# Performance work log

Measured on AMD Instinct MI355X. Metric: run time of the kernel, lower is better.

Reference implementation:

```python
import jax, jax.numpy as jnp
import numpy as np

B, T, IN_DIM, HID, H, L = 64, 256, 4096, 1024, 8, 2
HD = HID // H
K_TASK, K_ADP, OUT_DIM = 64, 1, 12
EPS = 1e-5


def _ln(x, g, b):
    m = x.mean(-1, keepdims=True)
    v = ((x - m) ** 2).mean(-1, keepdims=True)
    return (x - m) * jax.lax.rsqrt(v + EPS) * g + b


def _rope_tables(t_len, hd, base=10000.0):
    inv = 1.0 / base ** (jnp.arange(0, hd, 2, dtype=jnp.float32) / hd)
    freqs = jnp.arange(t_len, dtype=jnp.float32)[:, None] * inv[None, :]
    emb = jnp.concatenate([freqs, freqs], axis=-1)  # (T, hd)
    return jnp.cos(emb), jnp.sin(emb)


def _rotate_half(x):
    x1, x2 = x[..., ::2], x[..., 1::2]
    return jnp.stack((-x2, x1), axis=-1).reshape(x.shape)


def _apply_rope(q, k, cos, sin):
    cos = cos[None, None]
    sin = sin[None, None]
    return q * cos + _rotate_half(q) * sin, k * cos + _rotate_half(k) * sin


def _block(x, h_a_i, h_t_i, p, Wq, bq, Wks, bks, Wvs, bvs, Wka, bka, Wva, bva,
           Wkt, bkt, Wvt, bvt, Wo, bo, g, fg, fb, Wf, bff):
    Bx, Tx, C = x.shape
    gv = jnp.tanh(g)
    h_ad = jnp.concatenate([h_a_i, p], axis=1)  # (B, K_ADP+1, HID)
    cos, sin = _rope_tables(Tx, HD)

    def heads(t):
        return t.reshape(Bx, -1, H, HD).transpose(0, 2, 1, 3)

    q = heads(x @ Wq.T + bq)
    ks = heads(x @ Wks.T + bks)
    vs = heads(x @ Wvs.T + bvs)
    q, ks = _apply_rope(q, ks, cos, sin)
    ka = heads(h_ad @ Wka.T + bka)
    va = heads(h_ad @ Wva.T + bva)
    kt = heads(h_t_i @ Wkt.T + bkt)
    vt = heads(h_t_i @ Wvt.T + bvt)
    s_self = jnp.einsum('bhtd,bhsd->bhts', q, ks)
    s_ad = jnp.einsum('bhtd,bhsd->bhts', q, ka)
    s_tk = jnp.einsum('bhtd,bhsd->bhts', q, kt) * gv
    scores = jnp.concatenate([s_self, s_ad, s_tk], axis=-1) / np.float32(np.sqrt(HD))
    attn = jax.nn.softmax(scores, axis=-1)
    v_all = jnp.concatenate([vs, va, vt], axis=2)
    out = jnp.einsum('bhts,bhsd->bhtd', attn, v_all)
    out = out.transpose(0, 2, 1, 3).reshape(Bx, Tx, C)
    out = out @ Wo.T + bo
    return jax.nn.relu(_ln(out + x, fg, fb) @ Wf.T + bff)


def setup_inputs() -> dict:
    key = jax.random.key(0)
    kit = iter(jax.random.split(key, 64))
    def n(shape, s=0.02):
        return jax.random.normal(next(kit), shape, jnp.float32) * s
    return dict(
        x=jax.random.normal(next(kit), (B, T, IN_DIM), jnp.float32),
        h_a=jax.random.normal(next(kit), (B, L, K_ADP, HID), jnp.float32),
        h_t=jax.random.normal(next(kit), (B, L, K_TASK, HID), jnp.float32),
        p=jax.random.normal(next(kit), (B, 1, HID), jnp.float32),
        ln1_g=jnp.ones((IN_DIM,), jnp.float32), ln1_b=jnp.zeros((IN_DIM,), jnp.float32),
        W1=n((HID, IN_DIM)), b1=jnp.zeros((HID,), jnp.float32),
        Wq=n((L, HID, HID)), bq=jnp.zeros((L, HID), jnp.float32),
        Wks=n((L, HID, HID)), bks=jnp.zeros((L, HID), jnp.float32),
        Wvs=n((L, HID, HID)), bvs=jnp.zeros((L, HID), jnp.float32),
        Wka=n((L, HID, HID)), bka=jnp.zeros((L, HID), jnp.float32),
        Wva=n((L, HID, HID)), bva=jnp.zeros((L, HID), jnp.float32),
        Wkt=n((L, HID, HID)), bkt=jnp.zeros((L, HID), jnp.float32),
        Wvt=n((L, HID, HID)), bvt=jnp.zeros((L, HID), jnp.float32),
        Wo=n((L, HID, HID)), bo=jnp.zeros((L, HID), jnp.float32),
        gate=jnp.full((L,), 0.1, jnp.float32),
        fln_g=jnp.ones((L, HID), jnp.float32), fln_b=jnp.zeros((L, HID), jnp.float32),
        Wf=n((L, HID, HID)), bf=jnp.zeros((L, HID), jnp.float32),
        ln2_g=jnp.ones((HID,), jnp.float32), ln2_b=jnp.zeros((HID,), jnp.float32),
        W2=n((OUT_DIM, HID)), b2=jnp.zeros((OUT_DIM,), jnp.float32),
    )


def reference(x, h_a, h_t, p, ln1_g, ln1_b, W1, b1, Wq, bq, Wks, bks, Wvs, bvs,
              Wka, bka, Wva, bva, Wkt, bkt, Wvt, bvt, Wo, bo, gate, fln_g, fln_b,
              Wf, bf, ln2_g, ln2_b, W2, b2):
    h = _ln(x, ln1_g, ln1_b)
    h = jax.nn.relu(h @ W1.T + b1)  # (B, T, HID)
    for i in range(L):
        h = _block(h, h_a[:, i], h_t[:, i], p,
                   Wq[i], bq[i], Wks[i], bks[i], Wvs[i], bvs[i],
                   Wka[i], bka[i], Wva[i], bva[i], Wkt[i], bkt[i],
                   Wvt[i], bvt[i], Wo[i], bo[i], gate[i],
                   fln_g[i], fln_b[i], Wf[i], bf[i])
    h = _ln(h, ln2_g, ln2_b)
    return h @ W2.T + b2
```

## Files before the change

### kernel.cpp

```cpp
#include <hip/hip_runtime.h>
#include <hip/hip_bf16.h>
#include <cstdio>

typedef __hip_bfloat16 bf16;
typedef __attribute__((ext_vector_type(8))) short bf16x8;
typedef __attribute__((ext_vector_type(4))) float f32x4;

constexpr int NB = 64, NT = 256, NIN = 4096, NHID = 1024, NHEAD = 8, NHD = 128;
constexpr int NLAYER = 2, NKT = 64, NKEYS = 322, NOUT = 12;

__device__ __forceinline__ float bf2f(bf16 v) { return __bfloat162float(v); }
__device__ __forceinline__ bf16 f2bf(float v) { return __float2bfloat16(v); }

__device__ __forceinline__ void gload16(const void* g, void* l) {
  __builtin_amdgcn_global_load_lds((const __attribute__((address_space(1))) void*)g,
                                   (__attribute__((address_space(3))) void*)l, 16, 0, 0);
}

template <int OMODE, bool RELU>
__global__ __launch_bounds__(256) void gemm_bt(
    const bf16* __restrict__ A, const bf16* __restrict__ W,
    const float* __restrict__ bias, float* __restrict__ Cf,
    bf16* __restrict__ Cb, int M, int N, int K) {
  __shared__ bf16 As[128 * 32];
  __shared__ bf16 Bs[128 * 32];
  const int tid = threadIdx.x;
  const int wave = tid >> 6, lane = tid & 63;
  const int m0 = blockIdx.x * 128, n0 = blockIdx.y * 128;
  const int wm = (wave >> 1) * 64, wn = (wave & 1) * 64;
  const int lr = lane >> 4, lc = lane & 15;

  f32x4 acc[4][4];
#pragma unroll
  for (int i = 0; i < 4; ++i)
#pragma unroll
    for (int j = 0; j < 4; ++j) acc[i][j] = (f32x4){0.f, 0.f, 0.f, 0.f};

  for (int k0 = 0; k0 < K; k0 += 32) {
#pragma unroll
    for (int j = 0; j < 2; ++j) {
      const int c = (wave * 2 + j) * 64 + lane;
      const int row = c >> 2, kq = (c & 3) * 8;
      gload16(A + (size_t)(m0 + row) * K + k0 + kq, (char*)As + (size_t)(wave * 2 + j) * 1024);
      gload16(W + (size_t)(n0 + row) * K + k0 + kq, (char*)Bs + (size_t)(wave * 2 + j) * 1024);
    }
    __syncthreads();
    bf16x8 af[4], bv[4];
#pragma unroll
    for (int mi = 0; mi < 4; ++mi)
      af[mi] = *(const bf16x8*)(As + (wm + mi * 16 + lc) * 32 + lr * 8);
#pragma unroll
    for (int ni = 0; ni < 4; ++ni)
      bv[ni] = *(const bf16x8*)(Bs + (wn + ni * 16 + lc) * 32 + lr * 8);
#pragma unroll
    for (int mi = 0; mi < 4; ++mi)
#pragma unroll
      for (int ni = 0; ni < 4; ++ni)
        acc[mi][ni] = __builtin_amdgcn_mfma_f32_16x16x32_bf16(af[mi], bv[ni], acc[mi][ni], 0, 0, 0);
    __syncthreads();
  }

#pragma unroll
  for (int mi = 0; mi < 4; ++mi)
#pragma unroll
    for (int ni = 0; ni < 4; ++ni) {
      const int col = n0 + wn + ni * 16 + lc;
      const float bb = bias[col];
#pragma unroll
      for (int i = 0; i < 4; ++i) {
        const int row = m0 + wm + mi * 16 + lr * 4 + i;
        float v = acc[mi][ni][i] + bb;
        if (RELU) v = fmaxf(v, 0.f);
        if constexpr (OMODE == 0 || OMODE == 2) Cf[(size_t)row * N + col] = v;
        if constexpr (OMODE == 1 || OMODE == 2) Cb[(size_t)row * N + col] = f2bf(v);
      }
    }
}

template <int DIM, bool RES, bool OUTBF>
__global__ __launch_bounds__(256) void ln_kernel(
    const float* __restrict__ X, const float* __restrict__ R,
    const float* __restrict__ g, const float* __restrict__ bt,
    bf16* __restrict__ ob, float* __restrict__ of) {
  constexpr int PT = DIM / 1024;
  const int row = blockIdx.x, tid = threadIdx.x;
  const float4* xr = (const float4*)(X + (size_t)row * DIM);
  float4 v[PT];
  float s = 0.f, sq = 0.f;
#pragma unroll
  for (int j = 0; j < PT; ++j) {
    v[j] = xr[tid + j * 256];
    if constexpr (RES) {
      const float4 r4 = ((const float4*)(R + (size_t)row * DIM))[tid + j * 256];
      v[j].x += r4.x; v[j].y += r4.y; v[j].z += r4.z; v[j].w += r4.w;
    }
    s += v[j].x + v[j].y + v[j].z + v[j].w;
    sq += v[j].x * v[j].x + v[j].y * v[j].y + v[j].z * v[j].z + v[j].w * v[j].w;
  }
#pragma unroll
  for (int o = 32; o; o >>= 1) { s += __shfl_down(s, o); sq += __shfl_down(sq, o); }
  __shared__ float red[8];
  const int wave = tid >> 6, lane = tid & 63;
  if (!lane) { red[wave] = s; red[wave + 4] = sq; }
  __syncthreads();
  s = red[0] + red[1] + red[2] + red[3];
  sq = red[4] + red[5] + red[6] + red[7];
  const float mean = s * (1.f / DIM);
  const float var = sq * (1.f / DIM) - mean * mean;
  const float rs = rsqrtf(var + 1e-5f);
#pragma unroll
  for (int j = 0; j < PT; ++j) {
    const int c = (tid + j * 256) * 4;
    const float o0 = (v[j].x - mean) * rs * g[c + 0] + bt[c + 0];
    const float o1 = (v[j].y - mean) * rs * g[c + 1] + bt[c + 1];
    const float o2 = (v[j].z - mean) * rs * g[c + 2] + bt[c + 2];
    const float o3 = (v[j].w - mean) * rs * g[c + 3] + bt[c + 3];
    if constexpr (OUTBF) {
      union { bf16 h[4]; uint2 u; } t;
      t.h[0] = f2bf(o0); t.h[1] = f2bf(o1); t.h[2] = f2bf(o2); t.h[3] = f2bf(o3);
      ((uint2*)(ob + (size_t)row * DIM))[tid + j * 256] = t.u;
    } else {
      float4 w4 = {o0, o1, o2, o3};
      ((float4*)(of + (size_t)row * DIM))[tid + j * 256] = w4;
    }
  }
}

__global__ __launch_bounds__(256) void rope_tables(float* __restrict__ cT,
                                                   float* __restrict__ sT) {
  const int idx = blockIdx.x * 256 + threadIdx.x;
  if (idx >= NT * NHD) return;
  const int t = idx >> 7, d = idx & 127;
  const float inv = powf(10000.f, -(float)(d & 63) / 64.f);
  const float f = (float)t * inv;
  cT[idx] = cosf(f);
  sT[idx] = sinf(f);
}

__global__ __launch_bounds__(256) void rope_apply(bf16* __restrict__ q, bf16* __restrict__ k,
                                                  const float* __restrict__ cT,
                                                  const float* __restrict__ sT) {
  const int idx = blockIdx.x * 256 + threadIdx.x;
  const int i = idx & 63;
  const int hh = (idx >> 6) & 7;
  const int row = idx >> 9;
  const int t = row & (NT - 1);
  const size_t off = (size_t)row * NHID + hh * NHD + i * 2;
  const float c0 = cT[t * NHD + 2 * i], c1 = cT[t * NHD + 2 * i + 1];
  const float s0 = sT[t * NHD + 2 * i], s1 = sT[t * NHD + 2 * i + 1];
  union P2 { unsigned u; bf16 h[2]; };
  P2 a, o;
  a.u = *(const unsigned*)(q + off);
  float x0 = bf2f(a.h[0]), x1 = bf2f(a.h[1]);
  o.h[0] = f2bf(x0 * c0 - x1 * s0);
  o.h[1] = f2bf(x1 * c1 + x0 * s1);
  *(unsigned*)(q + off) = o.u;
  a.u = *(const unsigned*)(k + off);
  x0 = bf2f(a.h[0]); x1 = bf2f(a.h[1]);
  o.h[0] = f2bf(x0 * c0 - x1 * s0);
  o.h[1] = f2bf(x1 * c1 + x0 * s1);
  *(unsigned*)(k + off) = o.u;
}

__global__ __launch_bounds__(256) void attn_mfma(
    const bf16* __restrict__ qb, const bf16* __restrict__ ksb,
    const bf16* __restrict__ vsb, const bf16* __restrict__ kab,
    const bf16* __restrict__ vab, const bf16* __restrict__ ktb,
    const bf16* __restrict__ vtb, const float* __restrict__ gate, int layer,
    bf16* __restrict__ out) {
  __shared__ char Ks[64 * 256];
  __shared__ char Vts[128 * 128];
  __shared__ bf16 Pl[4][16][72];
  const int tid = threadIdx.x;
  const int w = tid >> 6, lane = tid & 63;
  const int lr = lane >> 4, lc = lane & 15;
  const int bid = blockIdx.x;
  const int qc = bid & 3, h = (bid >> 2) & 7, b = bid >> 5;
  const int q0 = qc * 64 + w * 16;
  const float gv = tanhf(gate[layer]);
  const float scale = 0.08838834764831845f;

  bf16x8 af[4];
#pragma unroll
  for (int ks_ = 0; ks_ < 4; ++ks_)
    af[ks_] = *(const bf16x8*)(qb + (size_t)(b * NT + q0 + lc) * NHID + h * NHD +
                               ks_ * 32 + lr * 8);

  f32x4 o[8];
#pragma unroll
  for (int n2 = 0; n2 < 8; ++n2) o[n2] = (f32x4){0.f, 0.f, 0.f, 0.f};
  float m_[4] = {-1e30f, -1e30f, -1e30f, -1e30f};
  float l_[4] = {0.f, 0.f, 0.f, 0.f};

  for (int kb = 0; kb < 6; ++kb) {
#pragma unroll
    for (int i = 0; i < 4; ++i) {
      const int c = tid + i * 256;
      const int key = c >> 4, d0 = (c & 15) * 8;
      const int gk = kb * 64 + key;
      const bf16 *ksrc, *vsrc;
      if (gk < 256) {
        const size_t r = (size_t)(b * NT + gk) * NHID;
        ksrc = ksb + r; vsrc = vsb + r;
      } else if (gk < 258) {
        const size_t r = (size_t)(b * 2 + (gk - 256)) * NHID;
        ksrc = kab + r; vsrc = vab + r;
      } else if (gk < NKEYS) {
        const size_t r = (size_t)(b * NKT + (gk - 258)) * NHID;
        ksrc = ktb + r; vsrc = vtb + r;
      } else {
        const size_t r = (size_t)(b * NT) * NHID;
        ksrc = ksb + r; vsrc = vsb + r;
      }
      const uint4 kv_ = *(const uint4*)(ksrc + h * NHD + d0);
      const uint4 vv_ = *(const uint4*)(vsrc + h * NHD + d0);
      *(uint4*)(Ks + key * 256 + ((d0 * 2) ^ ((key & 7) << 4))) = kv_;
      union { uint4 u; bf16 hh[8]; } t;
      t.u = vv_;
#pragma unroll
      for (int j = 0; j < 8; ++j) {
        const int d = d0 + j;
        *(bf16*)(Vts + d * 128 + ((key * 2) ^ ((d & 7) << 4))) = t.hh[j];
      }
    }
    __syncthreads();

    f32x4 s_[4];
#pragma unroll
    for (int n = 0; n < 4; ++n) s_[n] = (f32x4){0.f, 0.f, 0.f, 0.f};
#pragma unroll
    for (int n = 0; n < 4; ++n) {
      const int row = n * 16 + lc;
#pragma unroll
      for (int ks_ = 0; ks_ < 4; ++ks_) {
        const bf16x8 bk =
            *(const bf16x8*)(Ks + row * 256 + ((ks_ * 64 + lr * 16) ^ ((row & 7) << 4)));
        s_[n] = __builtin_amdgcn_mfma_f32_16x16x32_bf16(af[ks_], bk, s_[n], 0, 0, 0);
      }
    }
#pragma unroll
    for (int n = 0; n < 4; ++n) {
      const int gk = kb * 64 + n * 16 + lc;
      const float f = scale * (gk >= 258 ? gv : 1.f);
#pragma unroll
      for (int i = 0; i < 4; ++i)
        s_[n][i] = (gk >= NKEYS) ? -1e30f : s_[n][i] * f;
    }

    float corr[4];
#pragma unroll
    for (int i = 0; i < 4; ++i) {
      float mx = fmaxf(fmaxf(s_[0][i], s_[1][i]), fmaxf(s_[2][i], s_[3][i]));
#pragma unroll
      for (int off = 8; off; off >>= 1) mx = fmaxf(mx, __shfl_xor(mx, off));
      const float mnew = fmaxf(m_[i], mx);
      corr[i] = __expf(m_[i] - mnew);
      m_[i] = mnew;
      float rs = 0.f;
#pragma unroll
      for (int n = 0; n < 4; ++n) {
        const float p = __expf(s_[n][i] - mnew);
        s_[n][i] = p;
        rs += p;
      }
#pragma unroll
      for (int off = 8; off; off >>= 1) rs += __shfl_xor(rs, off);
      l_[i] = l_[i] * corr[i] + rs;
#pragma unroll
      for (int n = 0; n < 4; ++n) Pl[w][lr * 4 + i][n * 16 + lc] = f2bf(s_[n][i]);
    }
#pragma unroll
    for (int n2 = 0; n2 < 8; ++n2)
#pragma unroll
      for (int i = 0; i < 4; ++i) o[n2][i] *= corr[i];

    asm volatile("s_waitcnt lgkmcnt(0)" ::: "memory");

    const bf16x8 pa0 = *(const bf16x8*)(&Pl[w][lc][lr * 8]);
    const bf16x8 pa1 = *(const bf16x8*)(&Pl[w][lc][32 + lr * 8]);
#pragma unroll
    for (int n2 = 0; n2 < 8; ++n2) {
      const int row = n2 * 16 + lc;
      const bf16x8 bv0 =
          *(const bf16x8*)(Vts + row * 128 + ((lr * 16) ^ ((row & 7) << 4)));
      const bf16x8 bv1 =
          *(const bf16x8*)(Vts + row * 128 + ((64 + lr * 16) ^ ((row & 7) << 4)));
      o[n2] = __builtin_amdgcn_mfma_f32_16x16x32_bf16(pa0, bv0, o[n2], 0, 0, 0);
      o[n2] = __builtin_amdgcn_mfma_f32_16x16x32_bf16(pa1, bv1, o[n2], 0, 0, 0);
    }
    __syncthreads();
  }

#pragma unroll
  for (int i = 0; i < 4; ++i) {
    const float inv = 1.f / l_[i];
    bf16* op = out + (size_t)(b * NT + q0 + lr * 4 + i) * NHID + h * NHD;
#pragma unroll
    for (int n2 = 0; n2 < 8; ++n2) op[n2 * 16 + lc] = f2bf(o[n2][i] * inv);
  }
}

__global__ __launch_bounds__(256) void head_kernel(const float* __restrict__ lnf,
                                                   const float* __restrict__ W2,
                                                   const float* __restrict__ b2,
                                                   float* __restrict__ out) {
  __shared__ float4 xs[4096];
  const int r0 = blockIdx.x * 16;
  const float4* src = (const float4*)(lnf + (size_t)r0 * NHID);
  for (int e = threadIdx.x; e < 4096; e += 256) {
    const int row = e >> 8, c4 = e & 255;
    xs[c4 * 16 + row] = src[e];
  }
  __syncthreads();
  if (threadIdx.x < 192) {
    const int rr = threadIdx.x / 12, n = threadIdx.x % 12;
    const float4* w4 = (const float4*)(W2 + (size_t)n * NHID);
    float s = b2[n];
    for (int k = 0; k < 256; ++k) {
      const float4 a = xs[k * 16 + rr], w = w4[k];
      s += a.x * w.x + a.y * w.y + a.z * w.z + a.w * w.w;
    }
    out[(size_t)(r0 + rr) * NOUT + n] = s;
  }
}

__global__ __launch_bounds__(256) void cvt_f32_bf16(const float* __restrict__ in,
                                                    bf16* __restrict__ o, int n4) {
  const int i = blockIdx.x * 256 + threadIdx.x;
  if (i >= n4) return;
  const float4 v = ((const float4*)in)[i];
  union { bf16 h[4]; uint2 u; } t;
  t.h[0] = f2bf(v.x); t.h[1] = f2bf(v.y); t.h[2] = f2bf(v.z); t.h[3] = f2bf(v.w);
  ((uint2*)o)[i] = t.u;
}

__global__ __launch_bounds__(256) void cvt_ht(const float* __restrict__ ht, int layer,
                                              bf16* __restrict__ o) {
  const int i = blockIdx.x * 256 + threadIdx.x;
  if (i >= NB * NKT * NHID / 4) return;
  const int c4 = i & 255;
  const int s = (i >> 8) & 63;
  const int bb = i >> 14;
  const float4 v =
      ((const float4*)(ht + ((size_t)((bb * NLAYER + layer) * NKT + s)) * NHID))[c4];
  union { bf16 h[4]; uint2 u; } t;
  t.h[0] = f2bf(v.x); t.h[1] = f2bf(v.y); t.h[2] = f2bf(v.z); t.h[3] = f2bf(v.w);
  ((uint2*)o)[i] = t.u;
}

__global__ __launch_bounds__(256) void build_had(const float* __restrict__ ha,
                                                 const float* __restrict__ p, int layer,
                                                 bf16* __restrict__ o) {
  const int i = blockIdx.x * 256 + threadIdx.x;
  if (i >= NB * 2 * NHID / 4) return;
  const int c4 = i & 255;
  const int s = (i >> 8) & 1;
  const int bb = i >> 9;
  const float* base = s ? (p + (size_t)bb * NHID) : (ha + (size_t)(bb * NLAYER + layer) * NHID);
  const float4 v = ((const float4*)base)[c4];
  union { bf16 h[4]; uint2 u; } t;
  t.h[0] = f2bf(v.x); t.h[1] = f2bf(v.y); t.h[2] = f2bf(v.z); t.h[3] = f2bf(v.w);
  ((uint2*)o)[i] = t.u;
}

extern "C" void kernel_launch(void* const* d_in, const int* in_sizes, int n_in,
                              void* d_out, int out_size, void* d_ws, size_t ws_size,
                              hipStream_t stream) {
  const float* x = (const float*)d_in[0];
  const float* h_a = (const float*)d_in[1];
  const float* h_t = (const float*)d_in[2];
  const float* p = (const float*)d_in[3];
  const float* ln1g = (const float*)d_in[4];
  const float* ln1b = (const float*)d_in[5];
  const float* W1 = (const float*)d_in[6];
  const float* b1 = (const float*)d_in[7];
  const float* Wq = (const float*)d_in[8];
  const float* bq = (const float*)d_in[9];
  const float* Wks = (const float*)d_in[10];
  const float* bks = (const float*)d_in[11];
  const float* Wvs = (const float*)d_in[12];
  const float* bvs = (const float*)d_in[13];
  const float* Wka = (const float*)d_in[14];
  const float* bka = (const float*)d_in[15];
  const float* Wva = (const float*)d_in[16];
  const float* bva = (const float*)d_in[17];
  const float* Wkt = (const float*)d_in[18];
  const float* bkt = (const float*)d_in[19];
  const float* Wvt = (const float*)d_in[20];
  const float* bvt = (const float*)d_in[21];
  const float* Wo = (const float*)d_in[22];
  const float* bo = (const float*)d_in[23];
  const float* gate = (const float*)d_in[24];
  const float* flng = (const float*)d_in[25];
  const float* flnb = (const float*)d_in[26];
  const float* Wf = (const float*)d_in[27];
  const float* bff = (const float*)d_in[28];
  const float* ln2g = (const float*)d_in[29];
  const float* ln2b = (const float*)d_in[30];
  const float* W2 = (const float*)d_in[31];
  const float* b2 = (const float*)d_in[32];

  char* wsp = (char*)d_ws;
  size_t off = 0;
  auto alloc = [&](size_t bytes) -> void* {
    void* rp = wsp + off;
    off = (off + bytes + 255) & ~(size_t)255;
    return rp;
  };
  const size_t MT = (size_t)NB * NT;

  bf16* W1b = (bf16*)alloc((size_t)NHID * NIN * 2);
  bf16* Wqb = (bf16*)alloc((size_t)NLAYER * NHID * NHID * 2);
  bf16* Wksb = (bf16*)alloc((size_t)NLAYER * NHID * NHID * 2);
  bf16* Wvsb = (bf16*)alloc((size_t)NLAYER * NHID * NHID * 2);
  bf16* Wkab = (bf16*)alloc((size_t)NLAYER * NHID * NHID * 2);
  bf16* Wvab = (bf16*)alloc((size_t)NLAYER * NHID * NHID * 2);
  bf16* Wktb = (bf16*)alloc((size_t)NLAYER * NHID * NHID * 2);
  bf16* Wvtb = (bf16*)alloc((size_t)NLAYER * NHID * NHID * 2);
  bf16* Wob = (bf16*)alloc((size_t)NLAYER * NHID * NHID * 2);
  bf16* Wfb = (bf16*)alloc((size_t)NLAYER * NHID * NHID * 2);
  float* ropeC = (float*)alloc((size_t)NT * NHD * 4);
  float* ropeS = (float*)alloc((size_t)NT * NHD * 4);
  float* hF = (float*)alloc(MT * NHID * 4);
  bf16* hB = (bf16*)alloc(MT * NHID * 2);
  bf16* regA = (bf16*)alloc(MT * NIN * 2);
  float* oF = (float*)alloc(MT * NHID * 4);
  bf16* lnB = (bf16*)alloc(MT * NHID * 2);
  bf16* htiB = (bf16*)alloc((size_t)NB * NKT * NHID * 2);
  bf16* ktB = (bf16*)alloc((size_t)NB * NKT * NHID * 2);
  bf16* vtB = (bf16*)alloc((size_t)NB * NKT * NHID * 2);
  bf16* hadB = (bf16*)alloc((size_t)NB * 2 * NHID * 2);
  bf16* kaB = (bf16*)alloc((size_t)NB * 2 * NHID * 2);
  bf16* vaB = (bf16*)alloc((size_t)NB * 2 * NHID * 2);
  if (off > ws_size) {
    fprintf(stderr, "kernel_launch: ws too small (need %zu, have %zu)\n", off, ws_size);
    return;
  }

  bf16* h0b = regA;
  bf16* qB = regA;
  bf16* ksB = regA + MT * NHID;
  bf16* vsB = regA + 2 * MT * NHID;
  bf16* atB = regA + 3 * MT * NHID;

  cvt_f32_bf16<<<(NHID * NIN / 4) / 256, 256, 0, stream>>>(W1, W1b, NHID * NIN / 4);
  const int wn4 = NLAYER * NHID * NHID / 4;
  cvt_f32_bf16<<<wn4 / 256, 256, 0, stream>>>(Wq, Wqb, wn4);
  cvt_f32_bf16<<<wn4 / 256, 256, 0, stream>>>(Wks, Wksb, wn4);
  cvt_f32_bf16<<<wn4 / 256, 256, 0, stream>>>(Wvs, Wvsb, wn4);
  cvt_f32_bf16<<<wn4 / 256, 256, 0, stream>>>(Wka, Wkab, wn4);
  cvt_f32_bf16<<<wn4 / 256, 256, 0, stream>>>(Wva, Wvab, wn4);
  cvt_f32_bf16<<<wn4 / 256, 256, 0, stream>>>(Wkt, Wktb, wn4);
  cvt_f32_bf16<<<wn4 / 256, 256, 0, stream>>>(Wvt, Wvtb, wn4);
  cvt_f32_bf16<<<wn4 / 256, 256, 0, stream>>>(Wo, Wob, wn4);
  cvt_f32_bf16<<<wn4 / 256, 256, 0, stream>>>(Wf, Wfb, wn4);
  rope_tables<<<(NT * NHD + 255) / 256, 256, 0, stream>>>(ropeC, ropeS);

  ln_kernel<NIN, false, true><<<MT, 256, 0, stream>>>(x, nullptr, ln1g, ln1b, h0b, nullptr);
  gemm_bt<2, true><<<dim3(MT / 128, NHID / 128), 256, 0, stream>>>(
      h0b, W1b, b1, hF, hB, (int)MT, NHID, NIN);

  for (int li = 0; li < NLAYER; ++li) {
    const size_t wo_ = (size_t)li * NHID * NHID;
    build_had<<<(NB * 2 * NHID / 4) / 256, 256, 0, stream>>>(h_a, p, li, hadB);
    cvt_ht<<<(NB * NKT * NHID / 4) / 256, 256, 0, stream>>>(h_t, li, htiB);
    gemm_bt<1, false><<<dim3(MT / 128, 8), 256, 0, stream>>>(
        hB, Wqb + wo_, bq + li * NHID, nullptr, qB, (int)MT, NHID, NHID);
    gemm_bt<1, false><<<dim3(MT / 128, 8), 256, 0, stream>>>(
        hB, Wksb + wo_, bks + li * NHID, nullptr, ksB, (int)MT, NHID, NHID);
    gemm_bt<1, false><<<dim3(MT / 128, 8), 256, 0, stream>>>(
        hB, Wvsb + wo_, bvs + li * NHID, nullptr, vsB, (int)MT, NHID, NHID);
    gemm_bt<1, false><<<dim3(1, 8), 256, 0, stream>>>(
        hadB, Wkab + wo_, bka + li * NHID, nullptr, kaB, NB * 2, NHID, NHID);
    gemm_bt<1, false><<<dim3(1, 8), 256, 0, stream>>>(
        hadB, Wvab + wo_, bva + li * NHID, nullptr, vaB, NB * 2, NHID, NHID);
    gemm_bt<1, false><<<dim3(NB * NKT / 128, 8), 256, 0, stream>>>(
        htiB, Wktb + wo_, bkt + li * NHID, nullptr, ktB, NB * NKT, NHID, NHID);
    gemm_bt<1, false><<<dim3(NB * NKT / 128, 8), 256, 0, stream>>>(
        htiB, Wvtb + wo_, bvt + li * NHID, nullptr, vtB, NB * NKT, NHID, NHID);
    rope_apply<<<(int)(MT * NHID / 2 / 256), 256, 0, stream>>>(qB, ksB, ropeC, ropeS);
    attn_mfma<<<NB * NHEAD * 4, 256, 0, stream>>>(
        qB, ksB, vsB, kaB, vaB, ktB, vtB, gate, li, atB);
    gemm_bt<0, false><<<dim3(MT / 128, 8), 256, 0, stream>>>(
        atB, Wob + wo_, bo + li * NHID, oF, nullptr, (int)MT, NHID, NHID);
    ln_kernel<NHID, true, true><<<MT, 256, 0, stream>>>(
        oF, hF, flng + li * NHID, flnb + li * NHID, lnB, nullptr);
    gemm_bt<2, true><<<dim3(MT / 128, 8), 256, 0, stream>>>(
        lnB, Wfb + wo_, bff + li * NHID, hF, hB, (int)MT, NHID, NHID);
  }

  ln_kernel<NHID, false, false><<<MT, 256, 0, stream>>>(hF, nullptr, ln2g, ln2b, nullptr, oF);
  head_kernel<<<MT / 16, 256, 0, stream>>>(oF, W2, b2, (float*)d_out);
}
```

Before: 2.226 ms.

## Fuse Q/K/V and task/adapter K/V projections into concatenated-weight GEMMs

Concatenates Wq/Wks/Wvs into one 3072-wide weight, and Wkt/Wvt and Wka/Wva into 2048-wide weights, with packed biases. Each group becomes a single GEMM writing an interleaved output buffer, cutting launches and re-reads of the shared A operand. Rope and attention now index the interleaved layouts with strides of 3072 or 2048. This adds bias-packing and per-layer weight-conversion launches, and makes the attention loads strided rather than contiguous.

```diff
diff --git a/kernel.cpp b/kernel.cpp
--- a/kernel.cpp
+++ b/kernel.cpp
@@ -137,36 +137,34 @@
   sT[idx] = sinf(f);
 }
 
-__global__ __launch_bounds__(256) void rope_apply(bf16* __restrict__ q, bf16* __restrict__ k,
-                                                  const float* __restrict__ cT,
-                                                  const float* __restrict__ sT) {
+__global__ __launch_bounds__(256) void rope_apply2(bf16* __restrict__ qkv,
+                                                   const float* __restrict__ cT,
+                                                   const float* __restrict__ sT) {
   const int idx = blockIdx.x * 256 + threadIdx.x;
   const int i = idx & 63;
   const int hh = (idx >> 6) & 7;
   const int row = idx >> 9;
   const int t = row & (NT - 1);
-  const size_t off = (size_t)row * NHID + hh * NHD + i * 2;
+  const size_t off = (size_t)row * 3072 + hh * NHD + i * 2;
   const float c0 = cT[t * NHD + 2 * i], c1 = cT[t * NHD + 2 * i + 1];
   const float s0 = sT[t * NHD + 2 * i], s1 = sT[t * NHD + 2 * i + 1];
   union P2 { unsigned u; bf16 h[2]; };
   P2 a, o;
-  a.u = *(const unsigned*)(q + off);
+  a.u = *(const unsigned*)(qkv + off);
   float x0 = bf2f(a.h[0]), x1 = bf2f(a.h[1]);
   o.h[0] = f2bf(x0 * c0 - x1 * s0);
   o.h[1] = f2bf(x1 * c1 + x0 * s1);
-  *(unsigned*)(q + off) = o.u;
-  a.u = *(const unsigned*)(k + off);
+  *(unsigned*)(qkv + off) = o.u;
+  a.u = *(const unsigned*)(qkv + off + 1024);
   x0 = bf2f(a.h[0]); x1 = bf2f(a.h[1]);
   o.h[0] = f2bf(x0 * c0 - x1 * s0);
   o.h[1] = f2bf(x1 * c1 + x0 * s1);
-  *(unsigned*)(k + off) = o.u;
+  *(unsigned*)(qkv + off + 1024) = o.u;
 }
 
 __global__ __launch_bounds__(256) void attn_mfma(
-    const bf16* __restrict__ qb, const bf16* __restrict__ ksb,
-    const bf16* __restrict__ vsb, const bf16* __restrict__ kab,
-    const bf16* __restrict__ vab, const bf16* __restrict__ ktb,
-    const bf16* __restrict__ vtb, const float* __restrict__ gate, int layer,
+    const bf16* __restrict__ qkv, const bf16* __restrict__ kava,
+    const bf16* __restrict__ ktvt, const float* __restrict__ gate, int layer,
     bf16* __restrict__ out) {
   __shared__ char Ks[64 * 256];
   __shared__ char Vts[128 * 128];
@@ -183,7 +181,7 @@
   bf16x8 af[4];
 #pragma unroll
   for (int ks_ = 0; ks_ < 4; ++ks_)
-    af[ks_] = *(const bf16x8*)(qb + (size_t)(b * NT + q0 + lc) * NHID + h * NHD +
+    af[ks_] = *(const bf16x8*)(qkv + (size_t)(b * NT + q0 + lc) * 3072 + h * NHD +
                                ks_ * 32 + lr * 8);
 
   f32x4 o[8];
@@ -198,22 +196,17 @@
       const int c = tid + i * 256;
       const int key = c >> 4, d0 = (c & 15) * 8;
       const int gk = kb * 64 + key;
-      const bf16 *ksrc, *vsrc;
-      if (gk < 256) {
-        const size_t r = (size_t)(b * NT + gk) * NHID;
-        ksrc = ksb + r; vsrc = vsb + r;
-      } else if (gk < 258) {
-        const size_t r = (size_t)(b * 2 + (gk - 256)) * NHID;
-        ksrc = kab + r; vsrc = vab + r;
-      } else if (gk < NKEYS) {
-        const size_t r = (size_t)(b * NKT + (gk - 258)) * NHID;
-        ksrc = ktb + r; vsrc = vtb + r;
-      } else {
-        const size_t r = (size_t)(b * NT) * NHID;
-        ksrc = ksb + r; vsrc = vsb + r;
-      }
-      const uint4 kv_ = *(const uint4*)(ksrc + h * NHD + d0);
-      const uint4 vv_ = *(const uint4*)(vsrc + h * NHD + d0);
+      const bf16* ksrc;
+      if (gk < 256)
+        ksrc = qkv + (size_t)(b * NT + gk) * 3072 + 1024 + h * NHD + d0;
+      else if (gk < 258)
+        ksrc = kava + (size_t)(b * 2 + (gk - 256)) * 2048 + h * NHD + d0;
+      else if (gk < NKEYS)
+        ksrc = ktvt + (size_t)(b * NKT + (gk - 258)) * 2048 + h * NHD + d0;
+      else
+        ksrc = qkv + (size_t)(b * NT) * 3072 + 1024 + h * NHD + d0;
+      const uint4 kv_ = *(const uint4*)ksrc;
+      const uint4 vv_ = *(const uint4*)(ksrc + 1024);
       *(uint4*)(Ks + key * 256 + ((d0 * 2) ^ ((key & 7) << 4))) = kv_;
       union { uint4 u; bf16 hh[8]; } t;
       t.u = vv_;
@@ -332,6 +325,18 @@
   union { bf16 h[4]; uint2 u; } t;
   t.h[0] = f2bf(v.x); t.h[1] = f2bf(v.y); t.h[2] = f2bf(v.z); t.h[3] = f2bf(v.w);
   ((uint2*)o)[i] = t.u;
+}
+
+__global__ __launch_bounds__(256) void pack_bias(const float* __restrict__ a,
+                                                 const float* __restrict__ b,
+                                                 const float* __restrict__ c,
+                                                 float* __restrict__ dst, int per) {
+  const int idx = blockIdx.x * 256 + threadIdx.x;
+  if (idx >= NLAYER * per) return;
+  const int l = idx / per, j = idx % per;
+  const int sel = j >> 10;
+  const float* src = (sel == 0) ? a : (sel == 1) ? b : c;
+  dst[idx] = src[l * 1024 + (j & 1023)];
 }
 
 __global__ __launch_bounds__(256) void cvt_ht(const float* __restrict__ ht, int layer,
@@ -408,17 +413,17 @@
     return rp;
   };
   const size_t MT = (size_t)NB * NT;
+  const size_t WSZ = (size_t)NHID * NHID;
 
   bf16* W1b = (bf16*)alloc((size_t)NHID * NIN * 2);
-  bf16* Wqb = (bf16*)alloc((size_t)NLAYER * NHID * NHID * 2);
-  bf16* Wksb = (bf16*)alloc((size_t)NLAYER * NHID * NHID * 2);
-  bf16* Wvsb = (bf16*)alloc((size_t)NLAYER * NHID * NHID * 2);
-  bf16* Wkab = (bf16*)alloc((size_t)NLAYER * NHID * NHID * 2);
-  bf16* Wvab = (bf16*)alloc((size_t)NLAYER * NHID * NHID * 2);
-  bf16* Wktb = (bf16*)alloc((size_t)NLAYER * NHID * NHID * 2);
-  bf16* Wvtb = (bf16*)alloc((size_t)NLAYER * NHID * NHID * 2);
-  bf16* Wob = (bf16*)alloc((size_t)NLAYER * NHID * NHID * 2);
-  bf16* Wfb = (bf16*)alloc((size_t)NLAYER * NHID * NHID * 2);
+  bf16* Wqkvb = (bf16*)alloc((size_t)NLAYER * 3 * WSZ * 2);
+  bf16* Wktvtb = (bf16*)alloc((size_t)NLAYER * 2 * WSZ * 2);
+  bf16* Wkavab = (bf16*)alloc((size_t)NLAYER * 2 * WSZ * 2);
+  bf16* Wob = (bf16*)alloc((size_t)NLAYER * WSZ * 2);
+  bf16* Wfb = (bf16*)alloc((size_t)NLAYER * WSZ * 2);
+  float* bqkv = (float*)alloc((size_t)NLAYER * 3072 * 4);
+  float* bktvt = (float*)alloc((size_t)NLAYER * 2048 * 4);
+  float* bkava = (float*)alloc((size_t)NLAYER * 2048 * 4);
   float* ropeC = (float*)alloc((size_t)NT * NHD * 4);
   float* ropeS = (float*)alloc((size_t)NT * NHD * 4);
   float* hF = (float*)alloc(MT * NHID * 4);
@@ -427,33 +432,34 @@
   float* oF = (float*)alloc(MT * NHID * 4);
   bf16* lnB = (bf16*)alloc(MT * NHID * 2);
   bf16* htiB = (bf16*)alloc((size_t)NB * NKT * NHID * 2);
-  bf16* ktB = (bf16*)alloc((size_t)NB * NKT * NHID * 2);
-  bf16* vtB = (bf16*)alloc((size_t)NB * NKT * NHID * 2);
+  bf16* ktvtC = (bf16*)alloc((size_t)NB * NKT * 2048 * 2);
   bf16* hadB = (bf16*)alloc((size_t)NB * 2 * NHID * 2);
-  bf16* kaB = (bf16*)alloc((size_t)NB * 2 * NHID * 2);
-  bf16* vaB = (bf16*)alloc((size_t)NB * 2 * NHID * 2);
+  bf16* kavaC = (bf16*)alloc((size_t)NB * 2 * 2048 * 2);
   if (off > ws_size) {
     fprintf(stderr, "kernel_launch: ws too small (need %zu, have %zu)\n", off, ws_size);
     return;
   }
 
   bf16* h0b = regA;
-  bf16* qB = regA;
-  bf16* ksB = regA + MT * NHID;
-  bf16* vsB = regA + 2 * MT * NHID;
-  bf16* atB = regA + 3 * MT * NHID;
+  bf16* qkvC = regA;
+  bf16* atB = regA + MT * 3072;
 
   cvt_f32_bf16<<<(NHID * NIN / 4) / 256, 256, 0, stream>>>(W1, W1b, NHID * NIN / 4);
-  const int wn4 = NLAYER * NHID * NHID / 4;
-  cvt_f32_bf16<<<wn4 / 256, 256, 0, stream>>>(Wq, Wqb, wn4);
-  cvt_f32_bf16<<<wn4 / 256, 256, 0, stream>>>(Wks, Wksb, wn4);
-  cvt_f32_bf16<<<wn4 / 256, 256, 0, stream>>>(Wvs, Wvsb, wn4);
-  cvt_f32_bf16<<<wn4 / 256, 256, 0, stream>>>(Wka, Wkab, wn4);
-  cvt_f32_bf16<<<wn4 / 256, 256, 0, stream>>>(Wva, Wvab, wn4);
-  cvt_f32_bf16<<<wn4 / 256, 256, 0, stream>>>(Wkt, Wktb, wn4);
-  cvt_f32_bf16<<<wn4 / 256, 256, 0, stream>>>(Wvt, Wvtb, wn4);
-  cvt_f32_bf16<<<wn4 / 256, 256, 0, stream>>>(Wo, Wob, wn4);
-  cvt_f32_bf16<<<wn4 / 256, 256, 0, stream>>>(Wf, Wfb, wn4);
+  const int m4 = (int)(WSZ / 4);
+  for (int l = 0; l < NLAYER; ++l) {
+    cvt_f32_bf16<<<m4 / 256, 256, 0, stream>>>(Wq + l * WSZ, Wqkvb + (size_t)l * 3 * WSZ, m4);
+    cvt_f32_bf16<<<m4 / 256, 256, 0, stream>>>(Wks + l * WSZ, Wqkvb + (size_t)l * 3 * WSZ + WSZ, m4);
+    cvt_f32_bf16<<<m4 / 256, 256, 0, stream>>>(Wvs + l * WSZ, Wqkvb + (size_t)l * 3 * WSZ + 2 * WSZ, m4);
+    cvt_f32_bf16<<<m4 / 256, 256, 0, stream>>>(Wkt + l * WSZ, Wktvtb + (size_t)l * 2 * WSZ, m4);
+    cvt_f32_bf16<<<m4 / 256, 256, 0, stream>>>(Wvt + l * WSZ, Wktvtb + (size_t)l * 2 * WSZ + WSZ, m4);
+    cvt_f32_bf16<<<m4 / 256, 256, 0, stream>>>(Wka + l * WSZ, Wkavab + (size_t)l * 2 * WSZ, m4);
+    cvt_f32_bf16<<<m4 / 256, 256, 0, stream>>>(Wva + l * WSZ, Wkavab + (size_t)l * 2 * WSZ + WSZ, m4);
+    cvt_f32_bf16<<<m4 / 256, 256, 0, stream>>>(Wo + l * WSZ, Wob + (size_t)l * WSZ, m4);
+    cvt_f32_bf16<<<m4 / 256, 256, 0, stream>>>(Wf + l * WSZ, Wfb + (size_t)l * WSZ, m4);
+  }
+  pack_bias<<<(NLAYER * 3072 + 255) / 256, 256, 0, stream>>>(bq, bks, bvs, bqkv, 3072);
+  pack_bias<<<(NLAYER * 2048 + 255) / 256, 256, 0, stream>>>(bkt, bvt, nullptr, bktvt, 2048);
+  pack_bias<<<(NLAYER * 2048 + 255) / 256, 256, 0, stream>>>(bka, bva, nullptr, bkava, 2048);
   rope_tables<<<(NT * NHD + 255) / 256, 256, 0, stream>>>(ropeC, ropeS);
 
   ln_kernel<NIN, false, true><<<MT, 256, 0, stream>>>(x, nullptr, ln1g, ln1b, h0b, nullptr);
@@ -461,32 +467,25 @@
       h0b, W1b, b1, hF, hB, (int)MT, NHID, NIN);
 
   for (int li = 0; li < NLAYER; ++li) {
-    const size_t wo_ = (size_t)li * NHID * NHID;
     build_had<<<(NB * 2 * NHID / 4) / 256, 256, 0, stream>>>(h_a, p, li, hadB);
     cvt_ht<<<(NB * NKT * NHID / 4) / 256, 256, 0, stream>>>(h_t, li, htiB);
-    gemm_bt<1, false><<<dim3(MT / 128, 8), 256, 0, stream>>>(
-        hB, Wqb + wo_, bq + li * NHID, nullptr, qB, (int)MT, NHID, NHID);
-    gemm_bt<1, false><<<dim3(MT / 128, 8), 256, 0, stream>>>(
-        hB, Wksb + wo_, bks + li * NHID, nullptr, ksB, (int)MT, NHID, NHID);
-    gemm_bt<1, false><<<dim3(MT / 128, 8), 256, 0, stream>>>(
-        hB, Wvsb + wo_, bvs + li * NHID, nullptr, vsB, (int)MT, NHID, NHID);
-    gemm_bt<1, false><<<dim3(1, 8), 256, 0, stream>>>(
-        hadB, Wkab + wo_, bka + li * NHID, nullptr, kaB, NB * 2, NHID, NHID);
-    gemm_bt<1, false><<<dim3(1, 8), 256, 0, stream>>>(
-        hadB, Wvab + wo_, bva + li * NHID, nullptr, vaB, NB * 2, NHID, NHID);
-    gemm_bt<1, false><<<dim3(NB * NKT / 128, 8), 256, 0, stream>>>(
-        htiB, Wktb + wo_, bkt + li * NHID, nullptr, ktB, NB * NKT, NHID, NHID);
-    gemm_bt<1, false><<<dim3(NB * NKT / 128, 8), 256, 0, stream>>>(
-        htiB, Wvtb + wo_, bvt + li * NHID, nullptr, vtB, NB * NKT, NHID, NHID);
-    rope_apply<<<(int)(MT * NHID / 2 / 256), 256, 0, stream>>>(qB, ksB, ropeC, ropeS);
-    attn_mfma<<<NB * NHEAD * 4, 256, 0, stream>>>(
-        qB, ksB, vsB, kaB, vaB, ktB, vtB, gate, li, atB);
+    gemm_bt<1, false><<<dim3(MT / 128, 24), 256, 0, stream>>>(
+        hB, Wqkvb + (size_t)li * 3 * WSZ, bqkv + li * 3072, nullptr, qkvC,
+        (int)MT, 3072, NHID);
+    gemm_bt<1, false><<<dim3(NB * NKT / 128, 16), 256, 0, stream>>>(
+        htiB, Wktvtb + (size_t)li * 2 * WSZ, bktvt + li * 2048, nullptr, ktvtC,
+        NB * NKT, 2048, NHID);
+    gemm_bt<1, false><<<dim3(1, 16), 256, 0, stream>>>(
+        hadB, Wkavab + (size_t)li * 2 * WSZ, bkava + li * 2048, nullptr, kavaC,
+        NB * 2, 2048, NHID);
+    rope_apply2<<<(int)(MT * NHID / 2 / 256), 256, 0, stream>>>(qkvC, ropeC, ropeS);
+    attn_mfma<<<NB * NHEAD * 4, 256, 0, stream>>>(qkvC, kavaC, ktvtC, gate, li, atB);
     gemm_bt<0, false><<<dim3(MT / 128, 8), 256, 0, stream>>>(
-        atB, Wob + wo_, bo + li * NHID, oF, nullptr, (int)MT, NHID, NHID);
+        atB, Wob + (size_t)li * WSZ, bo + li * NHID, oF, nullptr, (int)MT, NHID, NHID);
     ln_kernel<NHID, true, true><<<MT, 256, 0, stream>>>(
         oF, hF, flng + li * NHID, flnb + li * NHID, lnB, nullptr);
     gemm_bt<2, true><<<dim3(MT / 128, 8), 256, 0, stream>>>(
-        lnB, Wfb + wo_, bff + li * NHID, hF, hB, (int)MT, NHID, NHID);
+        lnB, Wfb + (size_t)li * WSZ, bff + li * NHID, hF, hB, (int)MT, NHID, NHID);
   }
 
   ln_kernel<NHID, false, false><<<MT, 256, 0, stream>>>(hF, nullptr, ln2g, ln2b, nullptr, oF);
```

New measurement: 2.050 ms. 1.09x faster.
